# Kernel optimization log

Measured on AMD Instinct MI355X. Metric: run time of the kernel, lower is better.

The kernel has to match this reference:

```python
import jax, jax.numpy as jnp
import numpy as np

DIM = 4096
N_HEADS = 32
N_KV_HEADS = 8
HEAD_DIM = 128
EPS = 1e-6
SEQ = 2048
N_SEG = 4
SEG_LEN = SEQ // N_SEG


def setup_inputs() -> dict:
    key = jax.random.key(0)
    ks = jax.random.split(key, 6)
    s = 0.02
    x = jax.random.normal(ks[0], (1, SEQ, DIM), jnp.float32)
    wq = jax.random.normal(ks[1], (N_HEADS * HEAD_DIM, DIM), jnp.float32) * s
    wk = jax.random.normal(ks[2], (N_KV_HEADS * HEAD_DIM, DIM), jnp.float32) * s
    wv = jax.random.normal(ks[3], (N_KV_HEADS * HEAD_DIM, DIM), jnp.float32) * s
    wo = jax.random.normal(ks[4], (DIM, N_HEADS * HEAD_DIM), jnp.float32) * s
    q_norm_w = jnp.ones((HEAD_DIM,), jnp.float32)
    k_norm_w = jnp.ones((HEAD_DIM,), jnp.float32)
    # RoPE cache: [max_pos, head_dim//2, 2] = (cos, sin)
    inv_freq = 1.0 / (10000.0 ** (jnp.arange(0, HEAD_DIM // 2, dtype=jnp.float32) / (HEAD_DIM // 2)))
    t = jnp.arange(SEQ, dtype=jnp.float32)
    freqs = jnp.outer(t, inv_freq)  # [SEQ, hd/2]
    rope_cache = jnp.stack([jnp.cos(freqs), jnp.sin(freqs)], axis=-1)
    # packed varlen: 4 segments of 512, positions restart per segment
    positions = (jnp.arange(SEQ, dtype=jnp.int32) % SEG_LEN)[None, :]
    cu_seqlens = jnp.arange(N_SEG + 1, dtype=jnp.int32) * SEG_LEN
    return {"x": x, "wq": wq, "wk": wk, "wv": wv, "wo": wo,
            "q_norm_w": q_norm_w, "k_norm_w": k_norm_w,
            "rope_cache": rope_cache, "positions": positions,
            "cu_seqlens": cu_seqlens}


def _rms_norm(x, w):
    xf = x.astype(jnp.float32)
    var = jnp.mean(xf * xf, axis=-1, keepdims=True)
    return w * (xf * jax.lax.rsqrt(var + EPS))


def _apply_rope(x, rope_cache, positions):
    # x: [bs, S, h, hd]; rope_cache: [P, hd/2, 2]; positions: [bs, S]
    cs = rope_cache[positions]                    # [bs, S, hd/2, 2]
    cos = cs[..., 0][:, :, None, :]               # [bs, S, 1, hd/2]
    sin = cs[..., 1][:, :, None, :]
    half = x.shape[-1] // 2
    x1, x2 = x[..., :half], x[..., half:]
    return jnp.concatenate([x1 * cos - x2 * sin, x2 * cos + x1 * sin], axis=-1)


def reference(x, wq, wk, wv, wo, q_norm_w, k_norm_w, rope_cache, positions, cu_seqlens):
    bs, S, _ = x.shape
    n_rep = N_HEADS // N_KV_HEADS
    xq = (x @ wq.T).reshape(bs, S, N_HEADS, HEAD_DIM)
    xk = (x @ wk.T).reshape(bs, S, N_KV_HEADS, HEAD_DIM)
    xv = (x @ wv.T).reshape(bs, S, N_KV_HEADS, HEAD_DIM)
    xq = _rms_norm(xq, q_norm_w)
    xk = _rms_norm(xk, k_norm_w)
    xq = _apply_rope(xq, rope_cache, positions)
    xk = _apply_rope(xk, rope_cache, positions)
    # GQA: repeat kv heads
    xk = jnp.repeat(xk, n_rep, axis=2)
    xv = jnp.repeat(xv, n_rep, axis=2)
    q = xq.transpose(0, 2, 1, 3)  # [bs, h, S, hd]
    k = xk.transpose(0, 2, 1, 3)
    v = xv.transpose(0, 2, 1, 3)
    # varlen mask: causal within each packed segment
    idx = jnp.arange(S)
    seg = jnp.searchsorted(cu_seqlens, idx, side='right') - 1  # [S]
    mask = (seg[:, None] == seg[None, :]) & (idx[:, None] >= idx[None, :])
    scale = HEAD_DIM ** -0.5
    scores = jnp.einsum('bhqd,bhkd->bhqk', q, k) * scale
    scores = jnp.where(mask[None, None], scores, jnp.float32(-1e30))
    probs = jax.nn.softmax(scores, axis=-1)
    out = jnp.einsum('bhqk,bhkd->bhqd', probs, v)
    out = out.transpose(0, 2, 1, 3).reshape(bs, S, N_HEADS * HEAD_DIM)
    return out @ wo.T
```

## Files before the change

### kernel.cpp

```cpp
#include <hip/hip_runtime.h>

typedef __bf16 bf16_t;
typedef __bf16 bf16x8 __attribute__((ext_vector_type(8)));
typedef __bf16 bf16x4 __attribute__((ext_vector_type(4)));
typedef float f32x4 __attribute__((ext_vector_type(4)));

#define SEQL 2048
#define DIMM 4096
#define NH 32
#define NKV 8
#define HD 128

__device__ __forceinline__ void gl2lds16(const void* g, void* l) {
  __builtin_amdgcn_global_load_lds((__attribute__((address_space(1))) void*)g,
                                   (__attribute__((address_space(3))) void*)l,
                                   16, 0, 0);
}

__global__ __launch_bounds__(256) void cvt5_kernel(const float* __restrict__ s0,
                                                   const float* __restrict__ s1,
                                                   const float* __restrict__ s2,
                                                   const float* __restrict__ s3,
                                                   const float* __restrict__ s4,
                                                   bf16_t* __restrict__ dst) {
  const long base = (long)blockIdx.x * 4096;
  const float* s;
  long o;
  if (base < 8388608L)       { s = s0; o = base; }
  else if (base < 25165824L) { s = s1; o = base - 8388608L; }
  else if (base < 29360128L) { s = s2; o = base - 25165824L; }
  else if (base < 33554432L) { s = s3; o = base - 29360128L; }
  else                       { s = s4; o = base - 33554432L; }
  const long t4 = threadIdx.x * 4;
#pragma unroll
  for (int j = 0; j < 4; ++j) {
    const long e = t4 + j * 1024;
    float4 v = *(const float4*)(s + o + e);
    bf16x4 ov;
    ov[0] = (bf16_t)v.x; ov[1] = (bf16_t)v.y; ov[2] = (bf16_t)v.z; ov[3] = (bf16_t)v.w;
    *(bf16x4*)(dst + base + e) = ov;
  }
}

template <typename CT>
__global__ __launch_bounds__(256, 3) void gemm_bt_kernel(const bf16_t* __restrict__ A,
                                                         const bf16_t* __restrict__ B,
                                                         CT* __restrict__ C,
                                                         int N, int K, int npanel) {
  __shared__ bf16_t lA[128 * 64];
  __shared__ bf16_t lB[128 * 64];
  const int tid = threadIdx.x;
  const int lin = blockIdx.x;
  const int xcd = lin & 7, idx = lin >> 3;
  const int bm = (idx & 15) * 128;
  const int bn = ((idx >> 4) + xcd * npanel) * 128;
  const int lane = tid & 63, wave = tid >> 6;
  const int wm = (wave >> 1) * 64, wn = (wave & 1) * 64;
  const int lr = lane & 15, quad = lane >> 4;

  f32x4 acc[4][4];
#pragma unroll
  for (int mi = 0; mi < 4; ++mi)
#pragma unroll
    for (int ni = 0; ni < 4; ++ni)
      acc[mi][ni] = (f32x4){0.f, 0.f, 0.f, 0.f};

  long soff[4];
#pragma unroll
  for (int c = 0; c < 4; ++c) {
    const int s = tid + 256 * c;
    soff[c] = (long)(s >> 3) * K + (((s & 7) ^ ((s >> 3) & 7)) << 3);
  }
  const bf16_t* Abase = A + (long)bm * K;
  const bf16_t* Bbase = B + (long)bn * K;

  for (int k0 = 0; k0 < K; k0 += 64) {
    __syncthreads();
#pragma unroll
    for (int c = 0; c < 4; ++c) {
      gl2lds16(Abase + soff[c] + k0, lA + (tid + 256 * c) * 8);
      gl2lds16(Bbase + soff[c] + k0, lB + (tid + 256 * c) * 8);
    }
    __syncthreads();
#pragma unroll
    for (int ks = 0; ks < 2; ++ks) {
      bf16x8 af[4], bfr[4];
#pragma unroll
      for (int mi = 0; mi < 4; ++mi)
        af[mi] = *(const bf16x8*)&lA[(wm + mi * 16 + lr) * 64 + ((((ks << 2) | quad) ^ (lr & 7)) << 3)];
#pragma unroll
      for (int ni = 0; ni < 4; ++ni)
        bfr[ni] = *(const bf16x8*)&lB[(wn + ni * 16 + lr) * 64 + ((((ks << 2) | quad) ^ (lr & 7)) << 3)];
#pragma unroll
      for (int mi = 0; mi < 4; ++mi)
#pragma unroll
        for (int ni = 0; ni < 4; ++ni)
          acc[mi][ni] = __builtin_amdgcn_mfma_f32_16x16x32_bf16(af[mi], bfr[ni], acc[mi][ni], 0, 0, 0);
    }
  }

#pragma unroll
  for (int mi = 0; mi < 4; ++mi) {
    const int row = bm + wm + mi * 16 + quad * 4;
#pragma unroll
    for (int ni = 0; ni < 4; ++ni) {
      const int col = bn + wn + ni * 16 + lr;
      CT* cp = C + (long)row * N + col;
#pragma unroll
      for (int r = 0; r < 4; ++r) cp[(long)r * N] = (CT)acc[mi][ni][r];
    }
  }
}

__global__ __launch_bounds__(256) void rmsrope_kernel(const bf16_t* __restrict__ xf,
                                                      int rstride,
                                                      const float* __restrict__ nw,
                                                      const float* __restrict__ rope,
                                                      const int* __restrict__ pos,
                                                      bf16_t* __restrict__ out,
                                                      int H, float oscale) {
  const int wave = threadIdx.x >> 6, lane = threadIdx.x & 63;
  const int flat = blockIdx.x * 4 + wave;
  const int s = flat / H, h = flat - s * H;
  const bf16_t* xp = xf + (long)s * rstride + h * HD;
  float x1 = (float)xp[lane], x2 = (float)xp[lane + 64];
  float ss = x1 * x1 + x2 * x2;
#pragma unroll
  for (int off = 32; off > 0; off >>= 1) ss += __shfl_xor(ss, off, 64);
  const float sc = rsqrtf(ss * (1.0f / 128.0f) + 1e-6f) * oscale;
  const float n1 = x1 * sc * nw[lane];
  const float n2 = x2 * sc * nw[lane + 64];
  const int p = pos[s];
  const float c = rope[p * 128 + lane * 2];
  const float sn = rope[p * 128 + lane * 2 + 1];
  bf16_t* op = out + ((long)h * SEQL + s) * HD;
  op[lane] = (bf16_t)(n1 * c - n2 * sn);
  op[lane + 64] = (bf16_t)(n2 * c + n1 * sn);
}

__global__ __launch_bounds__(256) void vtrans_kernel(const bf16_t* __restrict__ vf,
                                                     int rstride,
                                                     bf16_t* __restrict__ vb) {
  __shared__ bf16_t lt[128 * 129];
  const int hk = blockIdx.x >> 4;
  const int s0 = (blockIdx.x & 15) * 128;
  const int t = threadIdx.x;
  for (int i = t; i < 128 * 128; i += 256) {
    const int sl = i >> 7, d = i & 127;
    lt[sl * 129 + d] = vf[(long)(s0 + sl) * rstride + hk * HD + d];
  }
  __syncthreads();
#pragma unroll
  for (int cc = 0; cc < 8; ++cc) {
    const int cidx = t + 256 * cc;
    const int d = cidx >> 4, sc = (cidx & 15) * 8;
    bf16x8 v;
#pragma unroll
    for (int j = 0; j < 8; ++j) v[j] = lt[(sc + j) * 129 + d];
    *(bf16x8*)(vb + ((long)hk * HD + d) * SEQL + s0 + sc) = v;
  }
}

#define CK 64
#define PSTR 72
__global__ __launch_bounds__(256) void attn_kernel(const bf16_t* __restrict__ Q,
                                                   const bf16_t* __restrict__ Kt,
                                                   const bf16_t* __restrict__ Vt,
                                                   bf16_t* __restrict__ O) {
  __shared__ bf16_t lK[CK * 128];
  __shared__ bf16_t lV[144 * CK];
  __shared__ bf16_t lP[128 * PSTR];
  const int lin = blockIdx.x;
  const int qb = (lin < 256) ? (3 - (lin & 1)) : (lin & 1);
  const int gh = (lin >> 1) & 127;
  const int h = gh & 31, g = gh >> 5;
  const int hk = h >> 2;
  const int tid = threadIdx.x, lane = tid & 63, wave = tid >> 6;
  const int lr = lane & 15, quad = lane >> 4;
  const int s_base = g * 512 + qb * 128;

  if (tid < 128) {
    bf16x8 one8;
#pragma unroll
    for (int j = 0; j < 8; ++j) one8[j] = (bf16_t)1.0f;
    *(bf16x8*)&lV[128 * CK + tid * 8] = one8;
  }

  bf16x8 qf[2][4];
  const bf16_t* Qp = Q + ((long)h * SEQL + s_base + wave * 32 + lr) * HD + quad * 8;
#pragma unroll
  for (int mi = 0; mi < 2; ++mi)
#pragma unroll
    for (int ks = 0; ks < 4; ++ks)
      qf[mi][ks] = *(const bf16x8*)(Qp + mi * 16 * HD + ks * 32);

  f32x4 oacc[2][9];
#pragma unroll
  for (int mi = 0; mi < 2; ++mi)
#pragma unroll
    for (int di = 0; di < 9; ++di) oacc[mi][di] = (f32x4){0.f, 0.f, 0.f, 0.f};

  const int nchunk = 2 * qb + 2;
  for (int c = 0; c < nchunk; ++c) {
    __syncthreads();
    {
      const bf16_t* Kg = Kt + ((long)hk * SEQL + g * 512 + c * CK) * HD;
      const bf16_t* Vg = Vt + (long)hk * HD * SEQL + g * 512 + c * CK;
#pragma unroll
      for (int cc = 0; cc < 4; ++cc) {
        const int i = tid + 256 * cc;
        gl2lds16(Kg + (long)(i >> 4) * HD + (i & 15) * 8, lK + i * 8);
        gl2lds16(Vg + (long)(i >> 3) * SEQL + (i & 7) * 8, lV + i * 8);
      }
    }
    __syncthreads();

    f32x4 sv[2][4];
#pragma unroll
    for (int mi = 0; mi < 2; ++mi)
#pragma unroll
      for (int ni = 0; ni < 4; ++ni) sv[mi][ni] = (f32x4){0.f, 0.f, 0.f, 0.f};
#pragma unroll
    for (int ks = 0; ks < 4; ++ks) {
#pragma unroll
      for (int ni = 0; ni < 4; ++ni) {
        const bf16x8 kf = *(const bf16x8*)&lK[(ni * 16 + lr) * 128 + ks * 32 + quad * 8];
        sv[0][ni] = __builtin_amdgcn_mfma_f32_16x16x32_bf16(qf[0][ks], kf, sv[0][ni], 0, 0, 0);
        sv[1][ni] = __builtin_amdgcn_mfma_f32_16x16x32_bf16(qf[1][ks], kf, sv[1][ni], 0, 0, 0);
      }
    }

#pragma unroll
    for (int mi = 0; mi < 2; ++mi)
#pragma unroll
      for (int ni = 0; ni < 4; ++ni)
#pragma unroll
        for (int r = 0; r < 4; ++r) {
          const int colseg = c * CK + ni * 16 + lr;
          const int rowseg = qb * 128 + wave * 32 + mi * 16 + quad * 4 + r;
          float p = exp2f(sv[mi][ni][r]);
          p = (colseg > rowseg) ? 0.f : p;
          lP[(wave * 32 + mi * 16 + quad * 4 + r) * PSTR + ni * 16 + lr] = (bf16_t)p;
        }
    __syncthreads();

#pragma unroll
    for (int ks = 0; ks < 2; ++ks) {
      const bf16x8 pf0 = *(const bf16x8*)&lP[(wave * 32 + lr) * PSTR + ks * 32 + quad * 8];
      const bf16x8 pf1 = *(const bf16x8*)&lP[(wave * 32 + 16 + lr) * PSTR + ks * 32 + quad * 8];
#pragma unroll
      for (int di = 0; di < 9; ++di) {
        const bf16x8 vfr = *(const bf16x8*)&lV[(di * 16 + lr) * CK + ks * 32 + quad * 8];
        oacc[0][di] = __builtin_amdgcn_mfma_f32_16x16x32_bf16(pf0, vfr, oacc[0][di], 0, 0, 0);
        oacc[1][di] = __builtin_amdgcn_mfma_f32_16x16x32_bf16(pf1, vfr, oacc[1][di], 0, 0, 0);
      }
    }
  }

#pragma unroll
  for (int mi = 0; mi < 2; ++mi)
#pragma unroll
    for (int r = 0; r < 4; ++r) {
      const float inv = 1.0f / oacc[mi][8][r];
      const int row = s_base + wave * 32 + mi * 16 + quad * 4 + r;
      bf16_t* opp = O + (long)row * DIMM + h * HD + lr;
#pragma unroll
      for (int di = 0; di < 8; ++di) opp[di * 16] = (bf16_t)(oacc[mi][di][r] * inv);
    }
}

extern "C" void kernel_launch(void* const* d_in, const int* in_sizes, int n_in,
                              void* d_out, int out_size, void* d_ws, size_t ws_size,
                              hipStream_t stream) {
  (void)in_sizes; (void)n_in; (void)out_size; (void)ws_size;
  const float* x    = (const float*)d_in[0];
  const float* wq   = (const float*)d_in[1];
  const float* wk   = (const float*)d_in[2];
  const float* wv   = (const float*)d_in[3];
  const float* wo   = (const float*)d_in[4];
  const float* qnw  = (const float*)d_in[5];
  const float* knw  = (const float*)d_in[6];
  const float* rope = (const float*)d_in[7];
  const int*   pos  = (const int*)d_in[8];
  float* out = (float*)d_out;

  char* ws = (char*)d_ws;
  size_t off = 0;
  auto alloc = [&](size_t b) { char* p = ws + off; off += (b + 255) & ~(size_t)255; return p; };
  bf16_t* xb    = (bf16_t*)alloc((size_t)SEQL * DIMM * 2);
  bf16_t* wqkvb = (bf16_t*)alloc((size_t)DIMM * DIMM * 2);
  alloc((size_t)NKV * HD * DIMM * 2);
  alloc((size_t)NKV * HD * DIMM * 2);
  bf16_t* wob   = (bf16_t*)alloc((size_t)DIMM * DIMM * 2);
  bf16_t* qkvb  = (bf16_t*)alloc((size_t)SEQL * 6144 * 2);
  bf16_t* Qb    = (bf16_t*)wqkvb;
  bf16_t* Kb    = Qb + (size_t)NH * SEQL * HD;
  bf16_t* Vb    = Kb + (size_t)NKV * SEQL * HD;
  bf16_t* attnb = xb;

  const float c1 = 0.08838834764831845f * 1.4426950408889634f;

  cvt5_kernel<<<dim3(12288), 256, 0, stream>>>(x, wq, wk, wv, wo, xb);
  gemm_bt_kernel<bf16_t><<<dim3(768), 256, 0, stream>>>(xb, wqkvb, qkvb, 6144, DIMM, 6);
  rmsrope_kernel<<<dim3(SEQL * NH / 4), 256, 0, stream>>>(qkvb, 6144, qnw, rope, pos, Qb, NH, c1);
  rmsrope_kernel<<<dim3(SEQL * NKV / 4), 256, 0, stream>>>(qkvb + 4096, 6144, knw, rope, pos, Kb, NKV, 1.0f);
  vtrans_kernel<<<dim3(NKV * 16), 256, 0, stream>>>(qkvb + 5120, 6144, Vb);
  attn_kernel<<<dim3(512), 256, 0, stream>>>(Qb, Kb, Vb, attnb);
  gemm_bt_kernel<float><<<dim3(512), 256, 0, stream>>>(attnb, wob, out, DIMM, DIMM, 4);
}
```

Baseline: 461.4 us.

## Fuse QK RMSNorm, RoPE and V transpose into the QKV GEMM epilogue

The QKV projection GEMM now writes its 128x128 output tile to shared memory and, in the epilogue, applies per-head RMSNorm, query scaling and RoPE for Q/K tiles, or transposes V tiles, writing directly into the head-major Q, K and Vt buffers. This removes the intermediate qkv buffer round trip through global memory and three separate kernel launches. The cost is a heavier epilogue with many registers per thread (64-element buffers), which may hurt occupancy or spill. Q/K/V also get their own workspace buffers instead of reusing the weight buffer.

```diff
diff --git a/kernel.cpp b/kernel.cpp
--- a/kernel.cpp
+++ b/kernel.cpp
@@ -42,6 +42,129 @@
   }
 }
 
+#define TS 136
+#define QSCALE (0.08838834764831845f * 1.4426950408889634f)
+__global__ __launch_bounds__(256, 3) void gemm_qkv_kernel(const bf16_t* __restrict__ A,
+                                                          const bf16_t* __restrict__ B,
+                                                          const float* __restrict__ qnw,
+                                                          const float* __restrict__ knw,
+                                                          const float* __restrict__ rope,
+                                                          const int* __restrict__ pos,
+                                                          bf16_t* __restrict__ Qb,
+                                                          bf16_t* __restrict__ Kb,
+                                                          bf16_t* __restrict__ Vb) {
+  __shared__ __align__(16) bf16_t smem[128 * TS];
+  bf16_t* lA = smem;
+  bf16_t* lB = smem + 8192;
+  const int K = DIMM, npanel = 6;
+  const int tid = threadIdx.x;
+  const int lin = blockIdx.x;
+  const int xcd = lin & 7, idx = lin >> 3;
+  const int bm = (idx & 15) * 128;
+  const int bn = ((idx >> 4) + xcd * npanel) * 128;
+  const int lane = tid & 63, wave = tid >> 6;
+  const int wm = (wave >> 1) * 64, wn = (wave & 1) * 64;
+  const int lr = lane & 15, quad = lane >> 4;
+
+  f32x4 acc[4][4];
+#pragma unroll
+  for (int mi = 0; mi < 4; ++mi)
+#pragma unroll
+    for (int ni = 0; ni < 4; ++ni)
+      acc[mi][ni] = (f32x4){0.f, 0.f, 0.f, 0.f};
+
+  long soff[4];
+#pragma unroll
+  for (int c = 0; c < 4; ++c) {
+    const int s = tid + 256 * c;
+    soff[c] = (long)(s >> 3) * K + (((s & 7) ^ ((s >> 3) & 7)) << 3);
+  }
+  const bf16_t* Abase = A + (long)bm * K;
+  const bf16_t* Bbase = B + (long)bn * K;
+
+  for (int k0 = 0; k0 < K; k0 += 64) {
+    __syncthreads();
+#pragma unroll
+    for (int c = 0; c < 4; ++c) {
+      gl2lds16(Abase + soff[c] + k0, lA + (tid + 256 * c) * 8);
+      gl2lds16(Bbase + soff[c] + k0, lB + (tid + 256 * c) * 8);
+    }
+    __syncthreads();
+#pragma unroll
+    for (int ks = 0; ks < 2; ++ks) {
+      bf16x8 af[4], bfr[4];
+#pragma unroll
+      for (int mi = 0; mi < 4; ++mi)
+        af[mi] = *(const bf16x8*)&lA[(wm + mi * 16 + lr) * 64 + ((((ks << 2) | quad) ^ (lr & 7)) << 3)];
+#pragma unroll
+      for (int ni = 0; ni < 4; ++ni)
+        bfr[ni] = *(const bf16x8*)&lB[(wn + ni * 16 + lr) * 64 + ((((ks << 2) | quad) ^ (lr & 7)) << 3)];
+#pragma unroll
+      for (int mi = 0; mi < 4; ++mi)
+#pragma unroll
+        for (int ni = 0; ni < 4; ++ni)
+          acc[mi][ni] = __builtin_amdgcn_mfma_f32_16x16x32_bf16(af[mi], bfr[ni], acc[mi][ni], 0, 0, 0);
+    }
+  }
+
+  __syncthreads();
+  bf16_t* tile = smem;
+#pragma unroll
+  for (int mi = 0; mi < 4; ++mi)
+#pragma unroll
+    for (int ni = 0; ni < 4; ++ni)
+#pragma unroll
+      for (int r = 0; r < 4; ++r)
+        tile[(wm + mi * 16 + quad * 4 + r) * TS + wn + ni * 16 + lr] = (bf16_t)acc[mi][ni][r];
+  __syncthreads();
+
+  if (bn < 5120) {
+    const bool isQ = bn < 4096;
+    const float* nwp = isQ ? qnw : knw;
+    const float osc = isQ ? QSCALE : 1.0f;
+    bf16_t* outp = isQ ? (Qb + (long)(bn >> 7) * SEQL * HD)
+                       : (Kb + (long)((bn - 4096) >> 7) * SEQL * HD);
+    const int r = tid >> 1, hf = tid & 1;
+    bf16x8 rowv[16];
+#pragma unroll
+    for (int j = 0; j < 16; ++j) rowv[j] = *(const bf16x8*)&tile[r * TS + j * 8];
+    float ss = 0.f;
+#pragma unroll
+    for (int j = 0; j < 16; ++j)
+#pragma unroll
+      for (int e = 0; e < 8; ++e) { const float f = (float)rowv[j][e]; ss += f * f; }
+    const float sc = rsqrtf(ss * (1.0f / 128.0f) + 1e-6f) * osc;
+    const int p = pos[bm + r];
+    const float* rp = rope + p * 128;
+    bf16_t obuf[64];
+#pragma unroll
+    for (int g = 0; g < 8; ++g) {
+#pragma unroll
+      for (int e = 0; e < 8; ++e) {
+        const int i = g * 8 + e;
+        const float2 cs = *(const float2*)(rp + 2 * i);
+        const float nlo = (float)rowv[i >> 3][i & 7] * sc * nwp[i];
+        const float nhi = (float)rowv[8 + (i >> 3)][i & 7] * sc * nwp[64 + i];
+        obuf[i] = (bf16_t)(hf ? (nhi * cs.x + nlo * cs.y) : (nlo * cs.x - nhi * cs.y));
+      }
+    }
+    bf16_t* op = outp + (long)(bm + r) * HD + hf * 64;
+#pragma unroll
+    for (int g = 0; g < 8; ++g) *(bf16x8*)(op + g * 8) = *(const bf16x8*)&obuf[g * 8];
+  } else {
+    const int hk = (bn - 5120) >> 7;
+    const int d = tid & 127, shalf = tid >> 7;
+    bf16_t* vp = Vb + ((long)hk * HD + d) * SEQL + bm + shalf * 64;
+#pragma unroll
+    for (int grp = 0; grp < 8; ++grp) {
+      bf16x8 t;
+#pragma unroll
+      for (int e = 0; e < 8; ++e) t[e] = tile[(shalf * 64 + grp * 8 + e) * TS + d];
+      *(bf16x8*)(vp + grp * 8) = t;
+    }
+  }
+}
+
 template <typename CT>
 __global__ __launch_bounds__(256, 3) void gemm_bt_kernel(const bf16_t* __restrict__ A,
                                                          const bf16_t* __restrict__ B,
@@ -109,55 +232,6 @@
 #pragma unroll
       for (int r = 0; r < 4; ++r) cp[(long)r * N] = (CT)acc[mi][ni][r];
     }
-  }
-}
-
-__global__ __launch_bounds__(256) void rmsrope_kernel(const bf16_t* __restrict__ xf,
-                                                      int rstride,
-                                                      const float* __restrict__ nw,
-                                                      const float* __restrict__ rope,
-                                                      const int* __restrict__ pos,
-                                                      bf16_t* __restrict__ out,
-                                                      int H, float oscale) {
-  const int wave = threadIdx.x >> 6, lane = threadIdx.x & 63;
-  const int flat = blockIdx.x * 4 + wave;
-  const int s = flat / H, h = flat - s * H;
-  const bf16_t* xp = xf + (long)s * rstride + h * HD;
-  float x1 = (float)xp[lane], x2 = (float)xp[lane + 64];
-  float ss = x1 * x1 + x2 * x2;
-#pragma unroll
-  for (int off = 32; off > 0; off >>= 1) ss += __shfl_xor(ss, off, 64);
-  const float sc = rsqrtf(ss * (1.0f / 128.0f) + 1e-6f) * oscale;
-  const float n1 = x1 * sc * nw[lane];
-  const float n2 = x2 * sc * nw[lane + 64];
-  const int p = pos[s];
-  const float c = rope[p * 128 + lane * 2];
-  const float sn = rope[p * 128 + lane * 2 + 1];
-  bf16_t* op = out + ((long)h * SEQL + s) * HD;
-  op[lane] = (bf16_t)(n1 * c - n2 * sn);
-  op[lane + 64] = (bf16_t)(n2 * c + n1 * sn);
-}
-
-__global__ __launch_bounds__(256) void vtrans_kernel(const bf16_t* __restrict__ vf,
-                                                     int rstride,
-                                                     bf16_t* __restrict__ vb) {
-  __shared__ bf16_t lt[128 * 129];
-  const int hk = blockIdx.x >> 4;
-  const int s0 = (blockIdx.x & 15) * 128;
-  const int t = threadIdx.x;
-  for (int i = t; i < 128 * 128; i += 256) {
-    const int sl = i >> 7, d = i & 127;
-    lt[sl * 129 + d] = vf[(long)(s0 + sl) * rstride + hk * HD + d];
-  }
-  __syncthreads();
-#pragma unroll
-  for (int cc = 0; cc < 8; ++cc) {
-    const int cidx = t + 256 * cc;
-    const int d = cidx >> 4, sc = (cidx & 15) * 8;
-    bf16x8 v;
-#pragma unroll
-    for (int j = 0; j < 8; ++j) v[j] = lt[(sc + j) * 129 + d];
-    *(bf16x8*)(vb + ((long)hk * HD + d) * SEQL + s0 + sc) = v;
   }
 }
 
@@ -292,19 +366,13 @@
   alloc((size_t)NKV * HD * DIMM * 2);
   alloc((size_t)NKV * HD * DIMM * 2);
   bf16_t* wob   = (bf16_t*)alloc((size_t)DIMM * DIMM * 2);
-  bf16_t* qkvb  = (bf16_t*)alloc((size_t)SEQL * 6144 * 2);
-  bf16_t* Qb    = (bf16_t*)wqkvb;
-  bf16_t* Kb    = Qb + (size_t)NH * SEQL * HD;
-  bf16_t* Vb    = Kb + (size_t)NKV * SEQL * HD;
+  bf16_t* Qb    = (bf16_t*)alloc((size_t)NH * SEQL * HD * 2);
+  bf16_t* Kb    = (bf16_t*)alloc((size_t)NKV * SEQL * HD * 2);
+  bf16_t* Vb    = (bf16_t*)alloc((size_t)NKV * SEQL * HD * 2);
   bf16_t* attnb = xb;
 
-  const float c1 = 0.08838834764831845f * 1.4426950408889634f;
-
   cvt5_kernel<<<dim3(12288), 256, 0, stream>>>(x, wq, wk, wv, wo, xb);
-  gemm_bt_kernel<bf16_t><<<dim3(768), 256, 0, stream>>>(xb, wqkvb, qkvb, 6144, DIMM, 6);
-  rmsrope_kernel<<<dim3(SEQL * NH / 4), 256, 0, stream>>>(qkvb, 6144, qnw, rope, pos, Qb, NH, c1);
-  rmsrope_kernel<<<dim3(SEQL * NKV / 4), 256, 0, stream>>>(qkvb + 4096, 6144, knw, rope, pos, Kb, NKV, 1.0f);
-  vtrans_kernel<<<dim3(NKV * 16), 256, 0, stream>>>(qkvb + 5120, 6144, Vb);
+  gemm_qkv_kernel<<<dim3(768), 256, 0, stream>>>(xb, wqkvb, qnw, knw, rope, pos, Qb, Kb, Vb);
   attn_kernel<<<dim3(512), 256, 0, stream>>>(Qb, Kb, Vb, attnb);
   gemm_bt_kernel<float><<<dim3(512), 256, 0, stream>>>(attnb, wob, out, DIMM, DIMM, 4);
 }
```

After: 446.3 us. 3.3% less time.
